# Kernel tuning notes

Hardware: AMD Instinct MI355X
Metric: run time of the kernel (lower is better)

## Reference

```python
import jax, jax.numpy as jnp
import numpy as np

HID, H, QR, KVR, DN, DR, DV = 2048, 20, 768, 512, 192, 64, 256
HEAD_DIM = DN + DR  # 256
EPS = 1e-5
THETA = 1000000.0
SCALE = 1.0 / np.sqrt(HEAD_DIM)


def rmsnorm(x, w):
    rms = jnp.sqrt(jnp.mean(x * x, axis=-1, keepdims=True) + EPS)
    return x / rms * w


def rope_apply(x, positions):
    # x: [B,S,H,DR], positions: [B,S] int
    inv_freq = 1.0 / (THETA ** (jnp.arange(0, DR, 2, dtype=jnp.float32) / DR))  # [DR/2]
    freqs = positions.astype(jnp.float32)[..., None] * inv_freq  # [B,S,DR/2]
    cos = jnp.cos(freqs)[:, :, None, :]  # [B,S,1,DR/2]
    sin = jnp.sin(freqs)[:, :, None, :]
    x1, x2 = x[..., ::2], x[..., 1::2]
    return jnp.concatenate([x1 * cos - x2 * sin, x1 * sin + x2 * cos], axis=-1)


def setup_inputs() -> dict:
    key = jax.random.key(0)
    ks = jax.random.split(key, 7)
    B, S = 1, 2048
    return {
        "x": jax.random.normal(ks[0], (B, S, HID), dtype=jnp.float32),
        "positions": jnp.tile(jnp.arange(S, dtype=jnp.int32)[None, :], (B, 1)),
        "q_a_w": jax.random.normal(ks[1], (QR, HID), dtype=jnp.float32) * 0.02,
        "q_b_w": jax.random.normal(ks[2], (H * HEAD_DIM, QR), dtype=jnp.float32) * 0.02,
        "kv_a_w": jax.random.normal(ks[3], (KVR + DR, HID), dtype=jnp.float32) * 0.02,
        "kv_b_w": jax.random.normal(ks[4], (H * (DN + DV), KVR), dtype=jnp.float32) * 0.02,
        "o_w": jax.random.normal(ks[5], (HID, H * DV), dtype=jnp.float32) * 0.02,
        "q_a_ln_w": jnp.ones((QR,), dtype=jnp.float32),
        "kv_a_ln_w": jnp.ones((KVR,), dtype=jnp.float32),
    }


def reference(x, positions, q_a_w, q_b_w, kv_a_w, kv_b_w, o_w, q_a_ln_w, kv_a_ln_w):
    B, S, _ = x.shape
    # Q: LoRA down -> RMSNorm -> up
    q = rmsnorm(x @ q_a_w.T, q_a_ln_w) @ q_b_w.T  # [B,S,H*HEAD_DIM]
    q = q.reshape(B, S, H, HEAD_DIM)
    # KV: compressed projection, split lora / rope-pe parts
    kv_c = x @ kv_a_w.T  # [B,S,KVR+DR]
    kv_lora, k_rope_pe = kv_c[..., :KVR], kv_c[..., KVR:]
    kv_exp = rmsnorm(kv_lora, kv_a_ln_w) @ kv_b_w.T  # [B,S,H*(DN+DV)]
    kv_exp = kv_exp.reshape(B, S, H, DN + DV)
    k_nope, v = kv_exp[..., :DN], kv_exp[..., DN:]
    k_rope = jnp.broadcast_to(k_rope_pe[:, :, None, :], (B, S, H, DR))
    q_nope, q_rope = q[..., :DN], q[..., DN:]
    q_rope = rope_apply(q_rope, positions)
    k_rope = rope_apply(k_rope, positions)
    qf = jnp.concatenate([q_nope, q_rope], axis=-1)  # [B,S,H,HEAD_DIM]
    kf = jnp.concatenate([k_nope, k_rope], axis=-1)
    # attention: manual matmul-softmax-matmul
    attn = jnp.einsum("bqhd,bkhd->bhqk", qf, kf) * SCALE
    attn = jax.nn.softmax(attn, axis=-1)
    out = jnp.einsum("bhqk,bkhd->bqhd", attn, v).reshape(B, S, H * DV)
    return out @ o_w.T
```

## Files before the change

kernel.cpp:

```cpp
#include <hip/hip_runtime.h>
#include <hip/hip_bf16.h>

#define HID 2048
#define NH 20
#define QR 768
#define KVR 512
#define DN 192
#define DR 64
#define DV 256
#define HD 256
#define S_LEN 2048
#define HKV 448
#define KV_N (NH * HKV)
#define Q_N (NH * HD)
#define O_N (NH * DV)
#define KVA_N (KVR + DR)
#define KVAP 640
#define QKVA (QR + KVAP)

typedef short bf16x8 __attribute__((ext_vector_type(8)));
typedef short bf16x4 __attribute__((ext_vector_type(4)));
typedef float f32x4 __attribute__((ext_vector_type(4)));

__device__ inline short f2bs(float f) {
  __hip_bfloat16 h = __float2bfloat16(f);
  return *reinterpret_cast<short*>(&h);
}
__device__ inline float bs2f(short s) {
  __hip_bfloat16 h = *reinterpret_cast<__hip_bfloat16*>(&s);
  return __bfloat162float(h);
}

__device__ inline void gload16(const void* g, void* l) {
  __builtin_amdgcn_global_load_lds((const __attribute__((address_space(1))) void*)g,
                                   (__attribute__((address_space(3))) void*)l, 16, 0, 0);
}

#define WAIT_LGKM0() asm volatile("s_waitcnt lgkmcnt(0)" ::: "memory")
#define WAIT_VM0() asm volatile("s_waitcnt vmcnt(0)" ::: "memory")

__global__ void f2b_kernel(const float* __restrict__ in, short* __restrict__ out, size_t n) {
  size_t i = (size_t)blockIdx.x * blockDim.x + threadIdx.x;
  size_t stride = (size_t)gridDim.x * blockDim.x;
  for (; i < n; i += stride) out[i] = f2bs(in[i]);
}

template <int OUT_BF16>
__global__ __launch_bounds__(256) void gemm128(const short* __restrict__ A,
                                               const short* __restrict__ B,
                                               void* __restrict__ Cp,
                                               int M, int N, int K) {
  __shared__ alignas(16) short As[128 * 64];
  __shared__ alignas(16) short Bs[128 * 64];
  int tid = threadIdx.x;
  int w = tid >> 6, l = tid & 63;
  int lr = l & 15, lg = l >> 4;
  int wr = w >> 1, wc = w & 1;
  int row0 = blockIdx.y * 128, col0 = blockIdx.x * 128;
  f32x4 acc[4][4] = {};
  for (int k0 = 0; k0 < K; k0 += 64) {
    if (k0) __syncthreads();
#pragma unroll
    for (int p = 0; p < 4; ++p) {
      int c = p * 256 + tid;
      int row = c >> 3;
      int sb = ((c & 7) * 16) ^ ((row & 7) << 4);
      gload16((const char*)A + ((size_t)(row0 + row) * K + k0) * 2 + sb, (char*)As + c * 16);
      gload16((const char*)B + ((size_t)(col0 + row) * K + k0) * 2 + sb, (char*)Bs + c * 16);
    }
    __syncthreads();
    bf16x8 af[4][2], bf[4][2];
#pragma unroll
    for (int m = 0; m < 4; ++m)
#pragma unroll
      for (int kk = 0; kk < 2; ++kk) {
        int ra = wr * 64 + m * 16 + lr;
        int rb = wc * 64 + m * 16 + lr;
        int cb = kk * 64 + lg * 16;
        af[m][kk] = *(const bf16x8*)((const char*)As + ra * 128 + (cb ^ ((ra & 7) << 4)));
        bf[m][kk] = *(const bf16x8*)((const char*)Bs + rb * 128 + (cb ^ ((rb & 7) << 4)));
      }
#pragma unroll
    for (int m = 0; m < 4; ++m)
#pragma unroll
      for (int n = 0; n < 4; ++n) {
        acc[m][n] = __builtin_amdgcn_mfma_f32_16x16x32_bf16(af[m][0], bf[n][0], acc[m][n], 0, 0, 0);
        acc[m][n] = __builtin_amdgcn_mfma_f32_16x16x32_bf16(af[m][1], bf[n][1], acc[m][n], 0, 0, 0);
      }
  }
#pragma unroll
  for (int m = 0; m < 4; ++m)
#pragma unroll
    for (int n = 0; n < 4; ++n)
#pragma unroll
      for (int r = 0; r < 4; ++r) {
        int row = row0 + wr * 64 + m * 16 + lg * 4 + r;
        int col = col0 + wc * 64 + n * 16 + lr;
        if (OUT_BF16)
          ((short*)Cp)[(size_t)row * N + col] = f2bs(acc[m][n][r]);
        else
          ((float*)Cp)[(size_t)row * N + col] = acc[m][n][r];
      }
}

__global__ __launch_bounds__(256) void gemm64(const short* __restrict__ A,
                                              const short* __restrict__ B,
                                              float* __restrict__ C,
                                              int M, int N, int K) {
  __shared__ alignas(16) short As[64 * 64];
  __shared__ alignas(16) short Bs[128 * 64];
  int tid = threadIdx.x;
  int w = tid >> 6, l = tid & 63;
  int lr = l & 15, lg = l >> 4;
  int wr = w >> 1, wc = w & 1;
  int row0 = blockIdx.y * 64, col0 = blockIdx.x * 128;
  f32x4 acc[2][4] = {};
  for (int k0 = 0; k0 < K; k0 += 64) {
    if (k0) __syncthreads();
#pragma unroll
    for (int p = 0; p < 2; ++p) {
      int c = p * 256 + tid;
      int row = c >> 3;
      int sb = ((c & 7) * 16) ^ ((row & 7) << 4);
      gload16((const char*)A + ((size_t)(row0 + row) * K + k0) * 2 + sb, (char*)As + c * 16);
    }
#pragma unroll
    for (int p = 0; p < 4; ++p) {
      int c = p * 256 + tid;
      int row = c >> 3;
      int sb = ((c & 7) * 16) ^ ((row & 7) << 4);
      gload16((const char*)B + ((size_t)(col0 + row) * K + k0) * 2 + sb, (char*)Bs + c * 16);
    }
    __syncthreads();
    bf16x8 af[2][2], bf[4][2];
#pragma unroll
    for (int m = 0; m < 2; ++m)
#pragma unroll
      for (int kk = 0; kk < 2; ++kk) {
        int ra = wr * 32 + m * 16 + lr;
        int cb = kk * 64 + lg * 16;
        af[m][kk] = *(const bf16x8*)((const char*)As + ra * 128 + (cb ^ ((ra & 7) << 4)));
      }
#pragma unroll
    for (int n = 0; n < 4; ++n)
#pragma unroll
      for (int kk = 0; kk < 2; ++kk) {
        int rb = wc * 64 + n * 16 + lr;
        int cb = kk * 64 + lg * 16;
        bf[n][kk] = *(const bf16x8*)((const char*)Bs + rb * 128 + (cb ^ ((rb & 7) << 4)));
      }
#pragma unroll
    for (int m = 0; m < 2; ++m)
#pragma unroll
      for (int n = 0; n < 4; ++n) {
        acc[m][n] = __builtin_amdgcn_mfma_f32_16x16x32_bf16(af[m][0], bf[n][0], acc[m][n], 0, 0, 0);
        acc[m][n] = __builtin_amdgcn_mfma_f32_16x16x32_bf16(af[m][1], bf[n][1], acc[m][n], 0, 0, 0);
      }
  }
#pragma unroll
  for (int m = 0; m < 2; ++m)
#pragma unroll
    for (int n = 0; n < 4; ++n)
#pragma unroll
      for (int r = 0; r < 4; ++r) {
        int row = row0 + wr * 32 + m * 16 + lg * 4 + r;
        int col = col0 + wc * 64 + n * 16 + lr;
        C[(size_t)row * N + col] = acc[m][n][r];
      }
}

__global__ __launch_bounds__(256) void rmsnorm_kernel(const float* __restrict__ in,
                                                      const float* __restrict__ w,
                                                      short* __restrict__ out,
                                                      int N, int in_stride, int out_stride) {
  int row = blockIdx.x;
  const float* x = in + (size_t)row * in_stride;
  float ss = 0.f;
  for (int i = threadIdx.x; i < N; i += 256) { float v = x[i]; ss += v * v; }
#pragma unroll
  for (int off = 32; off >= 1; off >>= 1) ss += __shfl_down(ss, off);
  __shared__ float red[4];
  if ((threadIdx.x & 63) == 0) red[threadIdx.x >> 6] = ss;
  __syncthreads();
  float tot = red[0] + red[1] + red[2] + red[3];
  float sc = rsqrtf(tot / (float)N + 1e-5f);
  short* o = out + (size_t)row * out_stride;
  for (int i = threadIdx.x; i < N; i += 256) o[i] = f2bs(x[i] * sc * w[i]);
}

__global__ void rope_table_kernel(const int* __restrict__ pos, float* __restrict__ ct,
                                  float* __restrict__ st) {
  int s = blockIdx.x * blockDim.x + threadIdx.x;
  if (s >= S_LEN) return;
  double p = (double)pos[s];
  for (int d = 0; d < 32; ++d) {
    double invf = exp(-((double)(2 * d) / 64.0) * log(1.0e6));
    double a = p * invf;
    ct[s * 32 + d] = (float)cos(a);
    st[s * 32 + d] = (float)sin(a);
  }
}

__global__ void rope_q_kernel(short* __restrict__ q, const float* __restrict__ ct,
                              const float* __restrict__ st) {
  int idx = blockIdx.x * blockDim.x + threadIdx.x;
  if (idx >= S_LEN * NH) return;
  int s = idx / NH, h = idx % NH;
  short* p = q + (size_t)s * Q_N + h * HD + DN;
  float x[64];
#pragma unroll
  for (int i = 0; i < 64; ++i) x[i] = bs2f(p[i]);
  const float* c = ct + s * 32;
  const float* sn = st + s * 32;
#pragma unroll
  for (int d = 0; d < 32; ++d) {
    float x1 = x[2 * d], x2 = x[2 * d + 1];
    p[d] = f2bs(x1 * c[d] - x2 * sn[d]);
    p[32 + d] = f2bs(x1 * sn[d] + x2 * c[d]);
  }
}

__global__ void rope_k_kernel(const float* __restrict__ base, const float* __restrict__ ct,
                              const float* __restrict__ st, short* __restrict__ kr) {
  int s = blockIdx.x * blockDim.x + threadIdx.x;
  if (s >= S_LEN) return;
  const float* x = base + (size_t)s * QKVA;
  const float* c = ct + s * 32;
  const float* sn = st + s * 32;
  short* o = kr + s * 64;
#pragma unroll
  for (int d = 0; d < 32; ++d) {
    float x1 = x[2 * d], x2 = x[2 * d + 1];
    o[d] = f2bs(x1 * c[d] - x2 * sn[d]);
    o[32 + d] = f2bs(x1 * sn[d] + x2 * c[d]);
  }
}

__global__ void kc_build(const short* __restrict__ kvx, const short* __restrict__ kr,
                         short* __restrict__ kc) {
  int idx = blockIdx.x * 256 + threadIdx.x;
  int h = idx >> 16;
  int r = idx & 65535;
  int s = r >> 5, c = r & 31;
  const short* src = (c < 24) ? kvx + (size_t)s * KV_N + h * HKV + c * 8
                              : kr + (size_t)s * 64 + (c - 24) * 8;
  *(bf16x8*)(kc + ((size_t)h * S_LEN + s) * HD + c * 8) = *(const bf16x8*)src;
}

__global__ __launch_bounds__(256) void vtrans(const short* __restrict__ kvx,
                                              short* __restrict__ vtg) {
  __shared__ short tile[64][65];
  int s0 = blockIdx.x * 64, d0 = blockIdx.y * 64, h = blockIdx.z;
  int tid = threadIdx.x;
#pragma unroll
  for (int p = 0; p < 2; ++p) {
    int s = p * 32 + (tid >> 3), dc = (tid & 7) * 8;
    bf16x8 v = *(const bf16x8*)(kvx + (size_t)(s0 + s) * KV_N + h * HKV + DN + d0 + dc);
#pragma unroll
    for (int j = 0; j < 8; ++j) tile[s][dc + j] = v[j];
  }
  __syncthreads();
#pragma unroll
  for (int p = 0; p < 2; ++p) {
    int d = p * 32 + (tid >> 3), sc = (tid & 7) * 8;
    bf16x4 a, b;
#pragma unroll
    for (int j = 0; j < 4; ++j) a[j] = tile[sc + j][d];
#pragma unroll
    for (int j = 0; j < 4; ++j) b[j] = tile[sc + 4 + j][d];
    int q1 = sc & 31, q2 = q1 + 4;
    int p1 = (q1 < 16) ? (q1 >> 2) * 8 : ((q1 - 16) >> 2) * 8 + 4;
    int p2 = (q2 < 16) ? (q2 >> 2) * 8 : ((q2 - 16) >> 2) * 8 + 4;
    int s = ((d & 15) >> 1) & 3;
    p1 = ((((p1 >> 3) ^ s)) << 3) | (p1 & 7);
    p2 = ((((p2 >> 3) ^ s)) << 3) | (p2 & 7);
    size_t rowbase = ((size_t)h * DV + d0 + d) * S_LEN + s0 + (sc & ~31);
    *(bf16x4*)(vtg + rowbase + p1) = a;
    *(bf16x4*)(vtg + rowbase + p2) = b;
  }
}

__global__ __launch_bounds__(256, 4) void attn8(const short* __restrict__ q,
                                                const short* __restrict__ kc,
                                                const short* __restrict__ vtg,
                                                short* __restrict__ out) {
  __shared__ alignas(16) short ks[2][32 * 256];
  __shared__ alignas(16) short vt[2][256 * 32];
  int bid = blockIdx.x;
  int swz = (bid & 7) * 80 + (bid >> 3);
  int h = swz >> 5, qblk = swz & 31;
  int tid = threadIdx.x;
  int w = tid >> 6, l = tid & 63;
  int lr = l & 15, lg = l >> 4;

  const char* kch = (const char*)(kc + (size_t)h * S_LEN * HD);
  const short* vth = vtg + (size_t)h * DV * S_LEN;

  int qrow = qblk * 64 + w * 16 + lr;
  const short* qbase = q + (size_t)qrow * Q_N + h * HD;
  bf16x8 qf[8];
#pragma unroll
  for (int kk = 0; kk < 8; ++kk) {
    bf16x8 v = *(const bf16x8*)(qbase + kk * 32 + lg * 8);
#pragma unroll
    for (int j = 0; j < 8; ++j) v[j] = f2bs(bs2f(v[j]) * 0.0625f);
    qf[kk] = v;
  }

  f32x4 acc[16] = {};
  float m = -3e38f;
  float lsum = 0.f;

  auto stage_k = [&](int buf, int key0) {
#pragma unroll
    for (int p = 0; p < 4; ++p) {
      int c = p * 256 + tid;
      int row = c >> 5;
      int sb = ((c & 31) * 16) ^ ((row & 7) << 4);
      gload16(kch + (size_t)(key0 + row) * 512 + sb, (char*)ks[buf] + c * 16);
    }
  };
  auto stage_v = [&](int buf, int key0) {
#pragma unroll
    for (int p = 0; p < 4; ++p) {
      int c = p * 256 + tid;
      int d = c >> 2, slot = c & 3;
      gload16(vth + (size_t)d * S_LEN + key0 + slot * 8, (char*)vt[buf] + c * 16);
    }
  };

  stage_k(0, 0);
  stage_v(0, 0);
  WAIT_VM0();
  __builtin_amdgcn_s_barrier();

  int sxor = (lr >> 1) & 3;

  for (int kb = 0; kb < S_LEN / 32; ++kb) {
    int cur = kb & 1;
    int key0 = kb * 32;
    if (kb + 1 < S_LEN / 32) {
      stage_k(cur ^ 1, key0 + 32);
      stage_v(cur ^ 1, key0 + 32);
    }

    f32x4 s0 = {}, s1 = {};
    __builtin_amdgcn_s_setprio(1);
#pragma unroll
    for (int kk = 0; kk < 8; ++kk) {
      int cb = kk * 64 + lg * 16;
      int sw = (lr & 7) << 4;
      bf16x8 k0 = *(const bf16x8*)((const char*)ks[cur] + lr * 512 + (cb ^ sw));
      bf16x8 k1 = *(const bf16x8*)((const char*)ks[cur] + (16 + lr) * 512 + (cb ^ sw));
      s0 = __builtin_amdgcn_mfma_f32_16x16x32_bf16(k0, qf[kk], s0, 0, 0, 0);
      s1 = __builtin_amdgcn_mfma_f32_16x16x32_bf16(k1, qf[kk], s1, 0, 0, 0);
    }
    __builtin_amdgcn_s_setprio(0);

    float mx = fmaxf(fmaxf(fmaxf(s0[0], s0[1]), fmaxf(s0[2], s0[3])),
                     fmaxf(fmaxf(s1[0], s1[1]), fmaxf(s1[2], s1[3])));
    mx = fmaxf(mx, __shfl_xor(mx, 16));
    mx = fmaxf(mx, __shfl_xor(mx, 32));
    bool grow = mx > m + 8.f;
    if (__any((int)grow)) {
      float mn = fmaxf(m, mx);
      float co = __expf(m - mn);
      m = mn;
      lsum *= co;
      float c0 = __shfl(co, (l & 48) | (lg * 4 + 0));
      float c1 = __shfl(co, (l & 48) | (lg * 4 + 1));
      float c2 = __shfl(co, (l & 48) | (lg * 4 + 2));
      float c3 = __shfl(co, (l & 48) | (lg * 4 + 3));
#pragma unroll
      for (int t = 0; t < 16; ++t) {
        acc[t][0] *= c0; acc[t][1] *= c1; acc[t][2] *= c2; acc[t][3] *= c3;
      }
    }
    float e0 = __expf(s0[0] - m), e1 = __expf(s0[1] - m);
    float e2 = __expf(s0[2] - m), e3 = __expf(s0[3] - m);
    float e4 = __expf(s1[0] - m), e5 = __expf(s1[1] - m);
    float e6 = __expf(s1[2] - m), e7 = __expf(s1[3] - m);
    float ts = ((e0 + e1) + (e2 + e3)) + ((e4 + e5) + (e6 + e7));
    ts += __shfl_xor(ts, 16);
    ts += __shfl_xor(ts, 32);
    lsum += ts;
    bf16x8 pa;
    pa[0] = f2bs(e0); pa[1] = f2bs(e1); pa[2] = f2bs(e2); pa[3] = f2bs(e3);
    pa[4] = f2bs(e4); pa[5] = f2bs(e5); pa[6] = f2bs(e6); pa[7] = f2bs(e7);

    __builtin_amdgcn_s_setprio(1);
#pragma unroll
    for (int t = 0; t < 16; ++t) {
      int d = t * 16 + lr;
      bf16x8 vf = *(const bf16x8*)((const char*)vt[cur] + d * 64 + ((lg ^ sxor) << 4));
      acc[t] = __builtin_amdgcn_mfma_f32_16x16x32_bf16(pa, vf, acc[t], 0, 0, 0);
    }
    __builtin_amdgcn_s_setprio(0);

    WAIT_VM0();
    __builtin_amdgcn_s_barrier();
  }

  float inv = 1.f / lsum;
  float i0 = __shfl(inv, (l & 48) | (lg * 4 + 0));
  float i1 = __shfl(inv, (l & 48) | (lg * 4 + 1));
  float i2 = __shfl(inv, (l & 48) | (lg * 4 + 2));
  float i3 = __shfl(inv, (l & 48) | (lg * 4 + 3));
#pragma unroll
  for (int t = 0; t < 16; ++t) {
    int row = qblk * 64 + w * 16 + lg * 4;
    int col = h * DV + t * 16 + lr;
    out[(size_t)(row + 0) * O_N + col] = f2bs(acc[t][0] * i0);
    out[(size_t)(row + 1) * O_N + col] = f2bs(acc[t][1] * i1);
    out[(size_t)(row + 2) * O_N + col] = f2bs(acc[t][2] * i2);
    out[(size_t)(row + 3) * O_N + col] = f2bs(acc[t][3] * i3);
  }
}

extern "C" void kernel_launch(void* const* d_in, const int* in_sizes, int n_in,
                              void* d_out, int out_size, void* d_ws, size_t ws_size,
                              hipStream_t stream) {
  const float* x       = (const float*)d_in[0];
  const int*   pos     = (const int*)d_in[1];
  const float* q_a_w   = (const float*)d_in[2];
  const float* q_b_w   = (const float*)d_in[3];
  const float* kv_a_w  = (const float*)d_in[4];
  const float* kv_b_w  = (const float*)d_in[5];
  const float* o_w     = (const float*)d_in[6];
  const float* q_a_ln  = (const float*)d_in[7];
  const float* kv_a_ln = (const float*)d_in[8];
  float* out = (float*)d_out;

  char* p = (char*)d_ws;
  auto alloc = [&](size_t bytes) {
    char* r = p;
    p += (bytes + 255) & ~(size_t)255;
    return r;
  };
  short* xb    = (short*)alloc((size_t)S_LEN * HID * 2);
  short* wcat  = (short*)alloc((size_t)QKVA * HID * 2);
  short* qbw   = (short*)alloc((size_t)Q_N * QR * 2);
  short* kvbw  = (short*)alloc((size_t)KV_N * KVR * 2);
  short* ow    = (short*)alloc((size_t)HID * O_N * 2);
  float* qkv   = (float*)alloc((size_t)S_LEN * QKVA * 4);
  short* q_ln  = (short*)alloc((size_t)S_LEN * QR * 2);
  short* qbuf  = (short*)alloc((size_t)S_LEN * Q_N * 2);
  short* kv_ln = (short*)alloc((size_t)S_LEN * KVR * 2);
  short* kvx   = (short*)alloc((size_t)S_LEN * KV_N * 2);
  short* kr    = (short*)alloc((size_t)S_LEN * 64 * 2);
  float* ct    = (float*)alloc((size_t)S_LEN * 32 * 4);
  float* st    = (float*)alloc((size_t)S_LEN * 32 * 4);
  short* ao    = (short*)alloc((size_t)S_LEN * O_N * 2);
  short* kcb   = (short*)alloc((size_t)NH * S_LEN * HD * 2);
  short* vtg   = (short*)alloc((size_t)NH * DV * S_LEN * 2);
  (void)ws_size; (void)n_in; (void)in_sizes; (void)out_size;

  auto cvt = [&](const float* in, short* o, size_t n) {
    size_t blocks = (n + 255) / 256;
    if (blocks > 2048) blocks = 2048;
    f2b_kernel<<<dim3((unsigned)blocks), dim3(256), 0, stream>>>(in, o, n);
  };
  cvt(x, xb, (size_t)S_LEN * HID);
  cvt(q_a_w, wcat, (size_t)QR * HID);
  cvt(kv_a_w, wcat + (size_t)QR * HID, (size_t)KVA_N * HID);
  hipMemsetAsync(wcat + (size_t)(QR + KVA_N) * HID, 0, (size_t)(KVAP - KVA_N) * HID * 2, stream);
  cvt(q_b_w, qbw, (size_t)Q_N * QR);
  cvt(kv_b_w, kvbw, (size_t)KV_N * KVR);
  cvt(o_w, ow, (size_t)HID * O_N);

  dim3 blk(256);
  gemm64<<<dim3(QKVA / 128, S_LEN / 64), blk, 0, stream>>>(xb, wcat, qkv, S_LEN, QKVA, HID);
  rmsnorm_kernel<<<dim3(S_LEN), blk, 0, stream>>>(qkv, q_a_ln, q_ln, QR, QKVA, QR);
  rmsnorm_kernel<<<dim3(S_LEN), blk, 0, stream>>>(qkv + QR, kv_a_ln, kv_ln, KVR, QKVA, KVR);
  gemm128<1><<<dim3(Q_N / 128, S_LEN / 128), blk, 0, stream>>>(q_ln, qbw, qbuf, S_LEN, Q_N, QR);
  gemm128<1><<<dim3(KV_N / 128, S_LEN / 128), blk, 0, stream>>>(kv_ln, kvbw, kvx, S_LEN, KV_N, KVR);
  rope_table_kernel<<<dim3(S_LEN / 256), blk, 0, stream>>>(pos, ct, st);
  rope_q_kernel<<<dim3((S_LEN * NH + 255) / 256), blk, 0, stream>>>(qbuf, ct, st);
  rope_k_kernel<<<dim3(S_LEN / 256), blk, 0, stream>>>(qkv + QR + KVR, ct, st, kr);
  kc_build<<<dim3(NH * S_LEN * 32 / 256), blk, 0, stream>>>(kvx, kr, kcb);
  vtrans<<<dim3(S_LEN / 64, DV / 64, NH), blk, 0, stream>>>(kvx, vtg);
  attn8<<<dim3(NH * S_LEN / 64), blk, 0, stream>>>(qbuf, kcb, vtg, ao);
  gemm64<<<dim3(HID / 128, S_LEN / 64), blk, 0, stream>>>(ao, ow, out, S_LEN, HID, O_N);
}
```

Before: 451.2 us.

## Vectorize elementwise kernels, fuse K assembly into attention, split-K output GEMM

Widens the conversion, rmsnorm and rope kernels to 16-byte vector loads and stores. Drops the kc_build kernel: the attention kernel now gathers K directly from kvx and the rotated-key buffer, removing one full copy of K. Splits the QK accumulation into two independent MFMA chains, drops the setprio hints, and replaces the output gemm64 with two split-K gemm128 launches plus an add kernel. This trades a separate K materialisation and small-tile output GEMM for extra fp32 partial buffers and one more elementwise pass.

```diff
diff --git a/kernel.cpp b/kernel.cpp
--- a/kernel.cpp
+++ b/kernel.cpp
@@ -36,18 +36,35 @@
                                    (__attribute__((address_space(3))) void*)l, 16, 0, 0);
 }
 
-#define WAIT_LGKM0() asm volatile("s_waitcnt lgkmcnt(0)" ::: "memory")
 #define WAIT_VM0() asm volatile("s_waitcnt vmcnt(0)" ::: "memory")
 
-__global__ void f2b_kernel(const float* __restrict__ in, short* __restrict__ out, size_t n) {
+__global__ void f2b_kernel(const float* __restrict__ in, short* __restrict__ out, size_t n8) {
   size_t i = (size_t)blockIdx.x * blockDim.x + threadIdx.x;
   size_t stride = (size_t)gridDim.x * blockDim.x;
-  for (; i < n; i += stride) out[i] = f2bs(in[i]);
+  for (; i < n8; i += stride) {
+    f32x4 a = *(const f32x4*)(in + i * 8);
+    f32x4 b = *(const f32x4*)(in + i * 8 + 4);
+    bf16x8 r;
+    r[0] = f2bs(a[0]); r[1] = f2bs(a[1]); r[2] = f2bs(a[2]); r[3] = f2bs(a[3]);
+    r[4] = f2bs(b[0]); r[5] = f2bs(b[1]); r[6] = f2bs(b[2]); r[7] = f2bs(b[3]);
+    *(bf16x8*)(out + i * 8) = r;
+  }
+}
+
+__global__ void addf_kernel(const float* __restrict__ a, const float* __restrict__ b,
+                            float* __restrict__ o, size_t n4) {
+  size_t i = (size_t)blockIdx.x * blockDim.x + threadIdx.x;
+  size_t stride = (size_t)gridDim.x * blockDim.x;
+  for (; i < n4; i += stride) {
+    f32x4 x = *(const f32x4*)(a + i * 4);
+    f32x4 y = *(const f32x4*)(b + i * 4);
+    *(f32x4*)(o + i * 4) = x + y;
+  }
 }
 
 template <int OUT_BF16>
-__global__ __launch_bounds__(256) void gemm128(const short* __restrict__ A,
-                                               const short* __restrict__ B,
+__global__ __launch_bounds__(256) void gemm128(const short* __restrict__ A, int lda,
+                                               const short* __restrict__ B, int ldb,
                                                void* __restrict__ Cp,
                                                int M, int N, int K) {
   __shared__ alignas(16) short As[128 * 64];
@@ -65,8 +82,8 @@
       int c = p * 256 + tid;
       int row = c >> 3;
       int sb = ((c & 7) * 16) ^ ((row & 7) << 4);
-      gload16((const char*)A + ((size_t)(row0 + row) * K + k0) * 2 + sb, (char*)As + c * 16);
-      gload16((const char*)B + ((size_t)(col0 + row) * K + k0) * 2 + sb, (char*)Bs + c * 16);
+      gload16((const char*)A + ((size_t)(row0 + row) * lda + k0) * 2 + sb, (char*)As + c * 16);
+      gload16((const char*)B + ((size_t)(col0 + row) * ldb + k0) * 2 + sb, (char*)Bs + c * 16);
     }
     __syncthreads();
     bf16x8 af[4][2], bf[4][2];
@@ -176,7 +193,10 @@
   int row = blockIdx.x;
   const float* x = in + (size_t)row * in_stride;
   float ss = 0.f;
-  for (int i = threadIdx.x; i < N; i += 256) { float v = x[i]; ss += v * v; }
+  for (int i = threadIdx.x * 4; i < N; i += 1024) {
+    f32x4 v = *(const f32x4*)(x + i);
+    ss += v[0] * v[0] + v[1] * v[1] + v[2] * v[2] + v[3] * v[3];
+  }
 #pragma unroll
   for (int off = 32; off >= 1; off >>= 1) ss += __shfl_down(ss, off);
   __shared__ float red[4];
@@ -185,7 +205,14 @@
   float tot = red[0] + red[1] + red[2] + red[3];
   float sc = rsqrtf(tot / (float)N + 1e-5f);
   short* o = out + (size_t)row * out_stride;
-  for (int i = threadIdx.x; i < N; i += 256) o[i] = f2bs(x[i] * sc * w[i]);
+  for (int i = threadIdx.x * 4; i < N; i += 1024) {
+    f32x4 v = *(const f32x4*)(x + i);
+    f32x4 g = *(const f32x4*)(w + i);
+    bf16x4 r;
+    r[0] = f2bs(v[0] * sc * g[0]); r[1] = f2bs(v[1] * sc * g[1]);
+    r[2] = f2bs(v[2] * sc * g[2]); r[3] = f2bs(v[3] * sc * g[3]);
+    *(bf16x4*)(o + i) = r;
+  }
 }
 
 __global__ void rope_table_kernel(const int* __restrict__ pos, float* __restrict__ ct,
@@ -207,44 +234,52 @@
   if (idx >= S_LEN * NH) return;
   int s = idx / NH, h = idx % NH;
   short* p = q + (size_t)s * Q_N + h * HD + DN;
+  bf16x8 v[8];
+#pragma unroll
+  for (int j = 0; j < 8; ++j) v[j] = *(const bf16x8*)(p + j * 8);
   float x[64];
 #pragma unroll
-  for (int i = 0; i < 64; ++i) x[i] = bs2f(p[i]);
+  for (int j = 0; j < 8; ++j)
+#pragma unroll
+    for (int k = 0; k < 8; ++k) x[j * 8 + k] = bs2f(v[j][k]);
   const float* c = ct + s * 32;
   const float* sn = st + s * 32;
+  bf16x8 o[8];
 #pragma unroll
   for (int d = 0; d < 32; ++d) {
+    float cd = c[d], sd = sn[d];
     float x1 = x[2 * d], x2 = x[2 * d + 1];
-    p[d] = f2bs(x1 * c[d] - x2 * sn[d]);
-    p[32 + d] = f2bs(x1 * sn[d] + x2 * c[d]);
-  }
+    o[d >> 3][d & 7] = f2bs(x1 * cd - x2 * sd);
+    o[4 + (d >> 3)][d & 7] = f2bs(x1 * sd + x2 * cd);
+  }
+#pragma unroll
+  for (int j = 0; j < 8; ++j) *(bf16x8*)(p + j * 8) = o[j];
 }
 
 __global__ void rope_k_kernel(const float* __restrict__ base, const float* __restrict__ ct,
                               const float* __restrict__ st, short* __restrict__ kr) {
   int s = blockIdx.x * blockDim.x + threadIdx.x;
   if (s >= S_LEN) return;
-  const float* x = base + (size_t)s * QKVA;
+  const float* xp = base + (size_t)s * QKVA;
+  float x[64];
+#pragma unroll
+  for (int j = 0; j < 16; ++j) {
+    f32x4 v = *(const f32x4*)(xp + j * 4);
+    x[j * 4] = v[0]; x[j * 4 + 1] = v[1]; x[j * 4 + 2] = v[2]; x[j * 4 + 3] = v[3];
+  }
   const float* c = ct + s * 32;
   const float* sn = st + s * 32;
-  short* o = kr + s * 64;
+  bf16x8 o[8];
 #pragma unroll
   for (int d = 0; d < 32; ++d) {
+    float cd = c[d], sd = sn[d];
     float x1 = x[2 * d], x2 = x[2 * d + 1];
-    o[d] = f2bs(x1 * c[d] - x2 * sn[d]);
-    o[32 + d] = f2bs(x1 * sn[d] + x2 * c[d]);
-  }
-}
-
-__global__ void kc_build(const short* __restrict__ kvx, const short* __restrict__ kr,
-                         short* __restrict__ kc) {
-  int idx = blockIdx.x * 256 + threadIdx.x;
-  int h = idx >> 16;
-  int r = idx & 65535;
-  int s = r >> 5, c = r & 31;
-  const short* src = (c < 24) ? kvx + (size_t)s * KV_N + h * HKV + c * 8
-                              : kr + (size_t)s * 64 + (c - 24) * 8;
-  *(bf16x8*)(kc + ((size_t)h * S_LEN + s) * HD + c * 8) = *(const bf16x8*)src;
+    o[d >> 3][d & 7] = f2bs(x1 * cd - x2 * sd);
+    o[4 + (d >> 3)][d & 7] = f2bs(x1 * sd + x2 * cd);
+  }
+  short* kp = kr + s * 64;
+#pragma unroll
+  for (int j = 0; j < 8; ++j) *(bf16x8*)(kp + j * 8) = o[j];
 }
 
 __global__ __launch_bounds__(256) void vtrans(const short* __restrict__ kvx,
@@ -280,8 +315,9 @@
   }
 }
 
-__global__ __launch_bounds__(256, 4) void attn8(const short* __restrict__ q,
-                                                const short* __restrict__ kc,
+__global__ __launch_bounds__(256, 4) void attn9(const short* __restrict__ q,
+                                                const short* __restrict__ kvx,
+                                                const short* __restrict__ kr,
                                                 const short* __restrict__ vtg,
                                                 short* __restrict__ out) {
   __shared__ alignas(16) short ks[2][32 * 256];
@@ -293,7 +329,6 @@
   int w = tid >> 6, l = tid & 63;
   int lr = l & 15, lg = l >> 4;
 
-  const char* kch = (const char*)(kc + (size_t)h * S_LEN * HD);
   const short* vth = vtg + (size_t)h * DV * S_LEN;
 
   int qrow = qblk * 64 + w * 16 + lr;
@@ -316,8 +351,11 @@
     for (int p = 0; p < 4; ++p) {
       int c = p * 256 + tid;
       int row = c >> 5;
-      int sb = ((c & 31) * 16) ^ ((row & 7) << 4);
-      gload16(kch + (size_t)(key0 + row) * 512 + sb, (char*)ks[buf] + c * 16);
+      int chunk = (c & 31) ^ (row & 7);
+      const short* src = (chunk < 24)
+          ? kvx + (size_t)(key0 + row) * KV_N + h * HKV + chunk * 8
+          : kr + (size_t)(key0 + row) * 64 + (chunk - 24) * 8;
+      gload16(src, (char*)ks[buf] + c * 16);
     }
   };
   auto stage_v = [&](int buf, int key0) {
@@ -344,18 +382,23 @@
       stage_v(cur ^ 1, key0 + 32);
     }
 
-    f32x4 s0 = {}, s1 = {};
-    __builtin_amdgcn_s_setprio(1);
-#pragma unroll
-    for (int kk = 0; kk < 8; ++kk) {
-      int cb = kk * 64 + lg * 16;
+    f32x4 s0a = {}, s0b = {}, s1a = {}, s1b = {};
+#pragma unroll
+    for (int kk = 0; kk < 8; kk += 2) {
       int sw = (lr & 7) << 4;
-      bf16x8 k0 = *(const bf16x8*)((const char*)ks[cur] + lr * 512 + (cb ^ sw));
-      bf16x8 k1 = *(const bf16x8*)((const char*)ks[cur] + (16 + lr) * 512 + (cb ^ sw));
-      s0 = __builtin_amdgcn_mfma_f32_16x16x32_bf16(k0, qf[kk], s0, 0, 0, 0);
-      s1 = __builtin_amdgcn_mfma_f32_16x16x32_bf16(k1, qf[kk], s1, 0, 0, 0);
-    }
-    __builtin_amdgcn_s_setprio(0);
+      int cb0 = kk * 64 + lg * 16;
+      int cb1 = (kk + 1) * 64 + lg * 16;
+      bf16x8 k0a = *(const bf16x8*)((const char*)ks[cur] + lr * 512 + (cb0 ^ sw));
+      bf16x8 k1a = *(const bf16x8*)((const char*)ks[cur] + (16 + lr) * 512 + (cb0 ^ sw));
+      bf16x8 k0b = *(const bf16x8*)((const char*)ks[cur] + lr * 512 + (cb1 ^ sw));
+      bf16x8 k1b = *(const bf16x8*)((const char*)ks[cur] + (16 + lr) * 512 + (cb1 ^ sw));
+      s0a = __builtin_amdgcn_mfma_f32_16x16x32_bf16(k0a, qf[kk], s0a, 0, 0, 0);
+      s1a = __builtin_amdgcn_mfma_f32_16x16x32_bf16(k1a, qf[kk], s1a, 0, 0, 0);
+      s0b = __builtin_amdgcn_mfma_f32_16x16x32_bf16(k0b, qf[kk + 1], s0b, 0, 0, 0);
+      s1b = __builtin_amdgcn_mfma_f32_16x16x32_bf16(k1b, qf[kk + 1], s1b, 0, 0, 0);
+    }
+    f32x4 s0 = s0a + s0b;
+    f32x4 s1 = s1a + s1b;
 
     float mx = fmaxf(fmaxf(fmaxf(s0[0], s0[1]), fmaxf(s0[2], s0[3])),
                      fmaxf(fmaxf(s1[0], s1[1]), fmaxf(s1[2], s1[3])));
@@ -388,14 +431,12 @@
     pa[0] = f2bs(e0); pa[1] = f2bs(e1); pa[2] = f2bs(e2); pa[3] = f2bs(e3);
     pa[4] = f2bs(e4); pa[5] = f2bs(e5); pa[6] = f2bs(e6); pa[7] = f2bs(e7);
 
-    __builtin_amdgcn_s_setprio(1);
 #pragma unroll
     for (int t = 0; t < 16; ++t) {
       int d = t * 16 + lr;
       bf16x8 vf = *(const bf16x8*)((const char*)vt[cur] + d * 64 + ((lg ^ sxor) << 4));
       acc[t] = __builtin_amdgcn_mfma_f32_16x16x32_bf16(pa, vf, acc[t], 0, 0, 0);
     }
-    __builtin_amdgcn_s_setprio(0);
 
     WAIT_VM0();
     __builtin_amdgcn_s_barrier();
@@ -451,14 +492,16 @@
   float* ct    = (float*)alloc((size_t)S_LEN * 32 * 4);
   float* st    = (float*)alloc((size_t)S_LEN * 32 * 4);
   short* ao    = (short*)alloc((size_t)S_LEN * O_N * 2);
-  short* kcb   = (short*)alloc((size_t)NH * S_LEN * HD * 2);
   short* vtg   = (short*)alloc((size_t)NH * DV * S_LEN * 2);
+  float* op0   = (float*)alloc((size_t)S_LEN * HID * 4);
+  float* op1   = (float*)alloc((size_t)S_LEN * HID * 4);
   (void)ws_size; (void)n_in; (void)in_sizes; (void)out_size;
 
   auto cvt = [&](const float* in, short* o, size_t n) {
-    size_t blocks = (n + 255) / 256;
+    size_t n8 = n / 8;
+    size_t blocks = (n8 + 255) / 256;
     if (blocks > 2048) blocks = 2048;
-    f2b_kernel<<<dim3((unsigned)blocks), dim3(256), 0, stream>>>(in, o, n);
+    f2b_kernel<<<dim3((unsigned)blocks), dim3(256), 0, stream>>>(in, o, n8);
   };
   cvt(x, xb, (size_t)S_LEN * HID);
   cvt(q_a_w, wcat, (size_t)QR * HID);
@@ -472,13 +515,19 @@
   gemm64<<<dim3(QKVA / 128, S_LEN / 64), blk, 0, stream>>>(xb, wcat, qkv, S_LEN, QKVA, HID);
   rmsnorm_kernel<<<dim3(S_LEN), blk, 0, stream>>>(qkv, q_a_ln, q_ln, QR, QKVA, QR);
   rmsnorm_kernel<<<dim3(S_LEN), blk, 0, stream>>>(qkv + QR, kv_a_ln, kv_ln, KVR, QKVA, KVR);
-  gemm128<1><<<dim3(Q_N / 128, S_LEN / 128), blk, 0, stream>>>(q_ln, qbw, qbuf, S_LEN, Q_N, QR);
-  gemm128<1><<<dim3(KV_N / 128, S_LEN / 128), blk, 0, stream>>>(kv_ln, kvbw, kvx, S_LEN, KV_N, KVR);
+  gemm128<1><<<dim3(Q_N / 128, S_LEN / 128), blk, 0, stream>>>(q_ln, QR, qbw, QR, qbuf,
+                                                               S_LEN, Q_N, QR);
+  gemm128<1><<<dim3(KV_N / 128, S_LEN / 128), blk, 0, stream>>>(kv_ln, KVR, kvbw, KVR, kvx,
+                                                                S_LEN, KV_N, KVR);
   rope_table_kernel<<<dim3(S_LEN / 256), blk, 0, stream>>>(pos, ct, st);
   rope_q_kernel<<<dim3((S_LEN * NH + 255) / 256), blk, 0, stream>>>(qbuf, ct, st);
   rope_k_kernel<<<dim3(S_LEN / 256), blk, 0, stream>>>(qkv + QR + KVR, ct, st, kr);
-  kc_build<<<dim3(NH * S_LEN * 32 / 256), blk, 0, stream>>>(kvx, kr, kcb);
   vtrans<<<dim3(S_LEN / 64, DV / 64, NH), blk, 0, stream>>>(kvx, vtg);
-  attn8<<<dim3(NH * S_LEN / 64), blk, 0, stream>>>(qbuf, kcb, vtg, ao);
-  gemm64<<<dim3(HID / 128, S_LEN / 64), blk, 0, stream>>>(ao, ow, out, S_LEN, HID, O_N);
-}
+  attn9<<<dim3(NH * S_LEN / 64), blk, 0, stream>>>(qbuf, kvx, kr, vtg, ao);
+  gemm128<0><<<dim3(HID / 128, S_LEN / 128), blk, 0, stream>>>(ao, O_N, ow, O_N, op0,
+                                                               S_LEN, HID, O_N / 2);
+  gemm128<0><<<dim3(HID / 128, S_LEN / 128), blk, 0, stream>>>(ao + O_N / 2, O_N,
+                                                               ow + O_N / 2, O_N, op1,
+                                                               S_LEN, HID, O_N / 2);
+  addf_kernel<<<dim3(2048), blk, 0, stream>>>(op0, op1, out, (size_t)S_LEN * HID / 4);
+}
```

After: 555.4 us. 23.1% more time.
